# Kernel optimization log

Hardware: AMD Instinct MI355X
Metric: run time of the kernel (lower is better)

Reference implementation:

```python
import jax, jax.numpy as jnp
import numpy as np

N = 100000
E = 800000
D_IN = 128
D_OUT = 128
EPS = 1e-5


def setup_inputs() -> dict:
    key = jax.random.key(0)
    k = jax.random.split(key, 7)
    x = jax.random.normal(k[0], (N, D_IN), dtype=jnp.float32)
    edge_index = jax.random.randint(k[1], (2, E), 0, N, dtype=jnp.int64)
    # kaiming_uniform(a=sqrt(5)) on [out,in] -> bound = 1/sqrt(in_dim)
    bound = 1.0 / np.sqrt(D_IN)
    W_self = jax.random.uniform(k[2], (D_OUT, D_IN), minval=-bound, maxval=bound, dtype=jnp.float32)
    W_neigh = jax.random.uniform(k[3], (D_OUT, D_IN), minval=-bound, maxval=bound, dtype=jnp.float32)
    bias = jnp.zeros((D_OUT,), dtype=jnp.float32)
    gamma = jnp.ones((D_OUT,), dtype=jnp.float32)
    beta = jnp.zeros((D_OUT,), dtype=jnp.float32)
    return {"x": x, "edge_index": edge_index, "W_self": W_self,
            "W_neigh": W_neigh, "bias": bias, "gamma": gamma, "beta": beta}


def reference(x, edge_index, W_self, W_neigh, bias, gamma, beta):
    src, dst = edge_index[0], edge_index[1]
    # mean neighbor aggregation: segment-sum of gathered features / clamped degree
    agg = jax.ops.segment_sum(x[src], dst, num_segments=N)          # [N, D_IN]
    deg = jax.ops.segment_sum(jnp.ones_like(dst, dtype=x.dtype), dst, num_segments=N)
    neigh_mean = agg / jnp.maximum(deg, 1.0)[:, None]
    # dual linear + bias + ReLU
    out = jnp.einsum('nd,od->no', x, W_self) + jnp.einsum('nd,od->no', neigh_mean, W_neigh) + bias
    h = jax.nn.relu(out)
    # LayerNorm over last dim
    mu = jnp.mean(h, axis=-1, keepdims=True)
    var = jnp.var(h, axis=-1, keepdims=True)
    return (h - mu) * jax.lax.rsqrt(var + EPS) * gamma + beta
```

## Files before the change

kernel.cpp:

```cpp
#include <hip/hip_runtime.h>
#include <hip/hip_bf16.h>

#define N_NODES 100000
#define E_EDGES 800000
#define LN_EPS 1e-5f

#define P_BLOCKS 256
#define EPB 3125
#define SLICE 64
#define NBK 1563
#define NBK_PAD 1792
#define OFFS_STRIDE 1564
#define QCAP 768
#define CONV_PER_BLOCK 12500
#define NBPAD 136

typedef __attribute__((ext_vector_type(4))) float f32x4;
typedef __attribute__((ext_vector_type(8))) short short8;

__device__ __forceinline__ unsigned short f2bf(float f) {
    __hip_bfloat16 h = __float2bfloat16(f);
    return *reinterpret_cast<unsigned short*>(&h);
}
__device__ __forceinline__ float bflo(unsigned int u) { return __uint_as_float(u << 16); }
__device__ __forceinline__ float bfhi(unsigned int u) { return __uint_as_float(u & 0xffff0000u); }

__global__ __launch_bounds__(256) void fill_part1(
    const float* __restrict__ x, const int* __restrict__ ei,
    const float* __restrict__ Wself, const float* __restrict__ Wneigh,
    unsigned short* __restrict__ xb, unsigned int* __restrict__ gstore,
    unsigned short* __restrict__ offs, unsigned short* __restrict__ Wswz)
{
    const int t = threadIdx.x, b = blockIdx.x;
    if (b >= P_BLOCKS) {
        const float4* x4 = reinterpret_cast<const float4*>(x);
        ushort4* xb4 = reinterpret_cast<ushort4*>(xb);
        const int j0 = (b - P_BLOCKS) * CONV_PER_BLOCK;
        for (int j = t; j < CONV_PER_BLOCK; j += 256) {
            float4 v = x4[j0 + j];
            ushort4 o;
            o.x = f2bf(v.x); o.y = f2bf(v.y); o.z = f2bf(v.z); o.w = f2bf(v.w);
            xb4[j0 + j] = o;
        }
        if (b == P_BLOCKS) {
            for (int idx = t; idx < 4096; idx += 256) {
                int kstep = idx >> 9, n = (idx >> 6) & 7, lane = idx & 63;
                int l16 = lane & 15, quad = lane >> 4;
                int c = n * 16 + l16;
                int kk = kstep * 32 + quad * 8;
                const float* sp = (kk < 128) ? (Wself + c * 128 + kk)
                                             : (Wneigh + c * 128 + kk - 128);
                float4 v0 = *reinterpret_cast<const float4*>(sp);
                float4 v1 = *reinterpret_cast<const float4*>(sp + 4);
                ushort4 o0, o1;
                o0.x = f2bf(v0.x); o0.y = f2bf(v0.y); o0.z = f2bf(v0.z); o0.w = f2bf(v0.w);
                o1.x = f2bf(v1.x); o1.y = f2bf(v1.y); o1.z = f2bf(v1.z); o1.w = f2bf(v1.w);
                *reinterpret_cast<ushort4*>(Wswz + idx * 8) = o0;
                *reinterpret_cast<ushort4*>(Wswz + idx * 8 + 4) = o1;
            }
        }
        return;
    }
    __shared__ unsigned long long eds[EPB];
    __shared__ unsigned int sorted_l[EPB];
    __shared__ int hist[NBK_PAD];
    __shared__ int starts[NBK_PAD + 1];
    __shared__ int partial[256];
    for (int i = t; i < NBK_PAD; i += 256) hist[i] = 0;
    __syncthreads();
    const int e0 = b * EPB;
    for (int i = t; i < EPB; i += 256) {
        unsigned src = (unsigned)ei[e0 + i];
        unsigned dst = (unsigned)ei[E_EDGES + e0 + i];
        unsigned bk = dst >> 6;
        eds[i] = ((unsigned long long)bk << 32) | (src << 6) | (dst & 63u);
        atomicAdd(&hist[bk], 1);
    }
    __syncthreads();
    int h[7], s = 0;
#pragma unroll
    for (int k = 0; k < 7; ++k) { h[k] = hist[t * 7 + k]; s += h[k]; }
    partial[t] = s;
    __syncthreads();
    for (int off = 1; off < 256; off <<= 1) {
        int v = (t >= off) ? partial[t - off] : 0;
        __syncthreads();
        partial[t] += v;
        __syncthreads();
    }
    int run = partial[t] - s;
#pragma unroll
    for (int k = 0; k < 7; ++k) { starts[t * 7 + k] = run; run += h[k]; }
    if (t == 255) starts[NBK_PAD] = run;
    __syncthreads();
    for (int i = t; i < NBK_PAD; i += 256) hist[i] = 0;
    __syncthreads();
    for (int i = t; i < EPB; i += 256) {
        unsigned long long u = eds[i];
        unsigned bk = (unsigned)(u >> 32);
        int p = starts[bk] + atomicAdd(&hist[bk], 1);
        sorted_l[p] = (unsigned int)u;
    }
    __syncthreads();
    for (int i = t; i < EPB; i += 256)
        gstore[b * EPB + i] = sorted_l[i];
    for (int i = t; i < OFFS_STRIDE; i += 256)
        offs[b * OFFS_STRIDE + i] = (unsigned short)starts[i];
}

__global__ __launch_bounds__(256) void agg_gemm(
    const unsigned int* __restrict__ gstore, const unsigned short* __restrict__ offs,
    const unsigned short* __restrict__ xb, const unsigned short* __restrict__ Wswz,
    const float* __restrict__ bias, const float* __restrict__ gamma,
    const float* __restrict__ beta, float* __restrict__ out)
{
    __shared__ unsigned short nbT[SLICE][NBPAD];
    __shared__ unsigned int sortedq[QCAP];
    __shared__ int cnt_l[SLICE];
    __shared__ int run_l[SLICE];
    __shared__ int qs_l[SLICE + 1];
    const int t = threadIdx.x, b = blockIdx.x;
    if (t < SLICE) { cnt_l[t] = 0; run_l[t] = 0; }
    __syncthreads();
    const int s0 = offs[t * OFFS_STRIDE + b];
    const int s1 = offs[t * OFFS_STRIDE + b + 1];
    const unsigned int* myrun = gstore + t * EPB;
    for (int j = s0; j < s1; ++j)
        atomicAdd(&cnt_l[myrun[j] & 63u], 1);
    __syncthreads();
    if (t < SLICE) {
        int inc = cnt_l[t];
        for (int off = 1; off < 64; off <<= 1) {
            int u = __shfl_up(inc, off);
            if (t >= off) inc += u;
        }
        qs_l[t + 1] = inc;
        if (t == 0) qs_l[0] = 0;
    }
    __syncthreads();
    for (int j = s0; j < s1; ++j) {
        unsigned rec = myrun[j];
        int p = qs_l[rec & 63u] + atomicAdd(&run_l[rec & 63u], 1);
        if (p < QCAP) sortedq[p] = rec;
    }
    __syncthreads();
    const int wave = t >> 6, lane = t & 63;
    const int subi = lane >> 4, chunk = lane & 15;
    const uint4* x4 = reinterpret_cast<const uint4*>(xb);
    for (int ln = wave * 16; ln < wave * 16 + 16; ++ln) {
        const int qb = qs_l[ln], cc = qs_l[ln + 1] - qb;
        float acc[8];
#pragma unroll
        for (int k = 0; k < 8; ++k) acc[k] = 0.f;
        for (int i = 0; i < cc; i += 4) {
            int idx = i + subi;
            if (idx < cc) {
                unsigned rec = sortedq[qb + idx];
                uint4 v = x4[(rec >> 6) * 16 + chunk];
                acc[0] += bflo(v.x); acc[1] += bfhi(v.x);
                acc[2] += bflo(v.y); acc[3] += bfhi(v.y);
                acc[4] += bflo(v.z); acc[5] += bfhi(v.z);
                acc[6] += bflo(v.w); acc[7] += bfhi(v.w);
            }
        }
#pragma unroll
        for (int k = 0; k < 8; ++k) {
            acc[k] += __shfl_xor(acc[k], 16);
            acc[k] += __shfl_xor(acc[k], 32);
        }
        if (subi == 0) {
            float inv = 1.0f / (float)(cc > 1 ? cc : 1);
            uint4 o;
            o.x = ((unsigned)f2bf(acc[1] * inv) << 16) | f2bf(acc[0] * inv);
            o.y = ((unsigned)f2bf(acc[3] * inv) << 16) | f2bf(acc[2] * inv);
            o.z = ((unsigned)f2bf(acc[5] * inv) << 16) | f2bf(acc[4] * inv);
            o.w = ((unsigned)f2bf(acc[7] * inv) << 16) | f2bf(acc[6] * inv);
            *reinterpret_cast<uint4*>(&nbT[ln][chunk * 8]) = o;
        }
    }
    __syncthreads();
    const int l16 = lane & 15, quad = lane >> 4;
    f32x4 gacc[8];
#pragma unroll
    for (int n = 0; n < 8; ++n) gacc[n] = (f32x4)0.f;
    const int row = b * SLICE + wave * 16 + l16;
    const int rowc = row < N_NODES ? row : N_NODES - 1;
    const short8* wsz = reinterpret_cast<const short8*>(Wswz);
#pragma unroll
    for (int kstep = 0; kstep < 8; ++kstep) {
        short8 a;
        if (kstep < 4)
            a = *reinterpret_cast<const short8*>(xb + rowc * 128 + kstep * 32 + quad * 8);
        else
            a = *reinterpret_cast<const short8*>(&nbT[wave * 16 + l16][(kstep - 4) * 32 + quad * 8]);
#pragma unroll
        for (int n = 0; n < 8; ++n) {
            short8 bb = wsz[(kstep * 8 + n) * 64 + lane];
            gacc[n] = __builtin_amdgcn_mfma_f32_16x16x32_bf16(a, bb, gacc[n], 0, 0, 0);
        }
    }
    float bia[8], gam[8], bet[8];
#pragma unroll
    for (int n = 0; n < 8; ++n) {
        int col = n * 16 + l16;
        bia[n] = bias[col]; gam[n] = gamma[col]; bet[n] = beta[col];
    }
#pragma unroll
    for (int r = 0; r < 4; ++r) {
        float h[8], s = 0.f, q = 0.f;
#pragma unroll
        for (int n = 0; n < 8; ++n) {
            float v = gacc[n][r] + bia[n];
            v = fmaxf(v, 0.f);
            h[n] = v; s += v; q += v * v;
        }
#pragma unroll
        for (int msk = 1; msk <= 8; msk <<= 1) {
            s += __shfl_xor(s, msk);
            q += __shfl_xor(q, msk);
        }
        const float mu = s * (1.f / 128.f);
        const float var = q * (1.f / 128.f) - mu * mu;
        const float rs = rsqrtf(var + LN_EPS);
        const int R = b * SLICE + wave * 16 + quad * 4 + r;
        if (R < N_NODES) {
#pragma unroll
            for (int n = 0; n < 8; ++n)
                out[R * 128 + n * 16 + l16] = (h[n] - mu) * rs * gam[n] + bet[n];
        }
    }
}

extern "C" void kernel_launch(void* const* d_in, const int* in_sizes, int n_in,
                              void* d_out, int out_size, void* d_ws, size_t ws_size,
                              hipStream_t stream) {
    const float* x      = (const float*)d_in[0];
    const int*   ei     = (const int*)d_in[1];
    const float* Wself  = (const float*)d_in[2];
    const float* Wneigh = (const float*)d_in[3];
    const float* bias   = (const float*)d_in[4];
    const float* gamma  = (const float*)d_in[5];
    const float* beta   = (const float*)d_in[6];
    float* out = (float*)d_out;

    char* ws = (char*)d_ws;
    unsigned short* xb = (unsigned short*)ws;
    unsigned int* gstore = (unsigned int*)(ws + 25600000);
    unsigned short* offs = (unsigned short*)(ws + 28800000);
    unsigned short* Wswz = (unsigned short*)(ws + 29601792);

    fill_part1<<<512, 256, 0, stream>>>(x, ei, Wself, Wneigh, xb, gstore, offs, Wswz);
    agg_gemm<<<NBK, 256, 0, stream>>>(gstore, offs, xb, Wswz, bias, gamma, beta, out);
}
```

Before: 213.0 us.

## Split GEMM tile by output columns per wave and widen x conversion grid

The GEMM epilogue now gives each wave 32 output columns across all 64 rows of the tile, where before each wave owned 16 rows across all 128 columns. Each wave therefore loads only its two weight fragments per k-step instead of eight, while A fragments are loaded once per row group. LayerNorm statistics now need a cross-wave reduction through shared memory (reusing the sortedq buffer) with an extra barrier. Separately, the fp32-to-bf16 conversion of x moves from 256 blocks with contiguous chunks to 1024 grid-strided blocks, giving more parallelism and coalesced access.

After: 202.3 us. -5.0%, faster.

```diff
diff --git a/kernel.cpp b/kernel.cpp
--- a/kernel.cpp
+++ b/kernel.cpp
@@ -12,7 +12,8 @@
 #define NBK_PAD 1792
 #define OFFS_STRIDE 1564
 #define QCAP 768
-#define CONV_PER_BLOCK 12500
+#define CONV_BLOCKS 1024
+#define CONV_TOTAL 3200000
 #define NBPAD 136
 
 typedef __attribute__((ext_vector_type(4))) float f32x4;
@@ -35,12 +36,11 @@
     if (b >= P_BLOCKS) {
         const float4* x4 = reinterpret_cast<const float4*>(x);
         ushort4* xb4 = reinterpret_cast<ushort4*>(xb);
-        const int j0 = (b - P_BLOCKS) * CONV_PER_BLOCK;
-        for (int j = t; j < CONV_PER_BLOCK; j += 256) {
-            float4 v = x4[j0 + j];
+        for (int j = (b - P_BLOCKS) * 256 + t; j < CONV_TOTAL; j += CONV_BLOCKS * 256) {
+            float4 v = x4[j];
             ushort4 o;
             o.x = f2bf(v.x); o.y = f2bf(v.y); o.z = f2bf(v.z); o.w = f2bf(v.w);
-            xb4[j0 + j] = o;
+            xb4[j] = o;
         }
         if (b == P_BLOCKS) {
             for (int idx = t; idx < 4096; idx += 256) {
@@ -180,53 +180,75 @@
     }
     __syncthreads();
     const int l16 = lane & 15, quad = lane >> 4;
-    f32x4 gacc[8];
-#pragma unroll
-    for (int n = 0; n < 8; ++n) gacc[n] = (f32x4)0.f;
-    const int row = b * SLICE + wave * 16 + l16;
-    const int rowc = row < N_NODES ? row : N_NODES - 1;
+    f32x4 gacc[4][2];
+#pragma unroll
+    for (int m = 0; m < 4; ++m) { gacc[m][0] = (f32x4)0.f; gacc[m][1] = (f32x4)0.f; }
+    int rowsg[4];
+#pragma unroll
+    for (int m = 0; m < 4; ++m) {
+        int r = b * SLICE + m * 16 + l16;
+        rowsg[m] = r < N_NODES ? r : N_NODES - 1;
+    }
     const short8* wsz = reinterpret_cast<const short8*>(Wswz);
 #pragma unroll
     for (int kstep = 0; kstep < 8; ++kstep) {
-        short8 a;
-        if (kstep < 4)
-            a = *reinterpret_cast<const short8*>(xb + rowc * 128 + kstep * 32 + quad * 8);
-        else
-            a = *reinterpret_cast<const short8*>(&nbT[wave * 16 + l16][(kstep - 4) * 32 + quad * 8]);
-#pragma unroll
-        for (int n = 0; n < 8; ++n) {
-            short8 bb = wsz[(kstep * 8 + n) * 64 + lane];
-            gacc[n] = __builtin_amdgcn_mfma_f32_16x16x32_bf16(a, bb, gacc[n], 0, 0, 0);
-        }
-    }
-    float bia[8], gam[8], bet[8];
-#pragma unroll
-    for (int n = 0; n < 8; ++n) {
-        int col = n * 16 + l16;
-        bia[n] = bias[col]; gam[n] = gamma[col]; bet[n] = beta[col];
-    }
-#pragma unroll
-    for (int r = 0; r < 4; ++r) {
-        float h[8], s = 0.f, q = 0.f;
-#pragma unroll
-        for (int n = 0; n < 8; ++n) {
-            float v = gacc[n][r] + bia[n];
-            v = fmaxf(v, 0.f);
-            h[n] = v; s += v; q += v * v;
-        }
-#pragma unroll
-        for (int msk = 1; msk <= 8; msk <<= 1) {
-            s += __shfl_xor(s, msk);
-            q += __shfl_xor(q, msk);
-        }
-        const float mu = s * (1.f / 128.f);
-        const float var = q * (1.f / 128.f) - mu * mu;
-        const float rs = rsqrtf(var + LN_EPS);
-        const int R = b * SLICE + wave * 16 + quad * 4 + r;
-        if (R < N_NODES) {
-#pragma unroll
-            for (int n = 0; n < 8; ++n)
-                out[R * 128 + n * 16 + l16] = (h[n] - mu) * rs * gam[n] + bet[n];
+        const short8 bfr0 = wsz[(kstep * 8 + wave * 2 + 0) * 64 + lane];
+        const short8 bfr1 = wsz[(kstep * 8 + wave * 2 + 1) * 64 + lane];
+#pragma unroll
+        for (int m = 0; m < 4; ++m) {
+            short8 a;
+            if (kstep < 4)
+                a = *reinterpret_cast<const short8*>(xb + rowsg[m] * 128 + kstep * 32 + quad * 8);
+            else
+                a = *reinterpret_cast<const short8*>(&nbT[m * 16 + l16][(kstep - 4) * 32 + quad * 8]);
+            gacc[m][0] = __builtin_amdgcn_mfma_f32_16x16x32_bf16(a, bfr0, gacc[m][0], 0, 0, 0);
+            gacc[m][1] = __builtin_amdgcn_mfma_f32_16x16x32_bf16(a, bfr1, gacc[m][1], 0, 0, 0);
+        }
+    }
+    float bia[2], gam[2], bet[2];
+#pragma unroll
+    for (int nn = 0; nn < 2; ++nn) {
+        int col = wave * 32 + nn * 16 + l16;
+        bia[nn] = bias[col]; gam[nn] = gamma[col]; bet[nn] = beta[col];
+    }
+    float* redS = reinterpret_cast<float*>(sortedq);
+    float* redQ = redS + 256;
+#pragma unroll
+    for (int m = 0; m < 4; ++m) {
+#pragma unroll
+        for (int r = 0; r < 4; ++r) {
+            float v0 = fmaxf(gacc[m][0][r] + bia[0], 0.f);
+            float v1 = fmaxf(gacc[m][1][r] + bia[1], 0.f);
+            gacc[m][0][r] = v0; gacc[m][1][r] = v1;
+            float s = v0 + v1, q = v0 * v0 + v1 * v1;
+#pragma unroll
+            for (int msk = 1; msk <= 8; msk <<= 1) {
+                s += __shfl_xor(s, msk);
+                q += __shfl_xor(q, msk);
+            }
+            if (l16 == 0) {
+                int Rl = m * 16 + quad * 4 + r;
+                redS[wave * 64 + Rl] = s;
+                redQ[wave * 64 + Rl] = q;
+            }
+        }
+    }
+    __syncthreads();
+#pragma unroll
+    for (int m = 0; m < 4; ++m) {
+#pragma unroll
+        for (int r = 0; r < 4; ++r) {
+            const int Rl = m * 16 + quad * 4 + r;
+            float s = redS[Rl] + redS[64 + Rl] + redS[128 + Rl] + redS[192 + Rl];
+            float q = redQ[Rl] + redQ[64 + Rl] + redQ[128 + Rl] + redQ[192 + Rl];
+            const float mu = s * (1.f / 128.f);
+            const float var = q * (1.f / 128.f) - mu * mu;
+            const float rs = rsqrtf(var + LN_EPS);
+            const int R = b * SLICE + Rl;
+            if (R < N_NODES) {
+                out[R * 128 + wave * 32 + l16]      = (gacc[m][0][r] - mu) * rs * gam[0] + bet[0];
+                out[R * 128 + wave * 32 + 16 + l16] = (gacc[m][1][r] - mu) * rs * gam[1] + bet[1];
+            }
         }
     }
 }
@@ -249,6 +271,6 @@
     unsigned short* offs = (unsigned short*)(ws + 28800000);
     unsigned short* Wswz = (unsigned short*)(ws + 29601792);
 
-    fill_part1<<<512, 256, 0, stream>>>(x, ei, Wself, Wneigh, xb, gstore, offs, Wswz);
+    fill_part1<<<P_BLOCKS + CONV_BLOCKS, 256, 0, stream>>>(x, ei, Wself, Wneigh, xb, gstore, offs, Wswz);
     agg_gemm<<<NBK, 256, 0, stream>>>(gstore, offs, xb, Wswz, bias, gamma, beta, out);
 }
```
